# Kernel optimization log

Measured on AMD Instinct MI355X. Metric: run time of the kernel, lower is better.

The kernel has to match this reference:

```python
import jax, jax.numpy as jnp
import numpy as np

BATCH, CHANNELS, WINDOW, N_PATCHES = 16, 64, 200, 30
D_MODEL = 256
HIDDEN = D_MODEL // 2  # 128


def setup_inputs() -> dict:
    key = jax.random.key(0)
    ks = jax.random.split(key, 7)
    s = 1.0 / np.sqrt(HIDDEN)
    return {
        "x": jax.random.normal(ks[0], (BATCH, CHANNELS, WINDOW, N_PATCHES), dtype=jnp.float32),
        "W_ih": jax.random.normal(ks[1], (4 * HIDDEN, CHANNELS), dtype=jnp.float32) * s,
        "W_hh": jax.random.normal(ks[2], (4 * HIDDEN, HIDDEN), dtype=jnp.float32) * s,
        "b_ih": jax.random.normal(ks[3], (4 * HIDDEN,), dtype=jnp.float32) * s,
        "b_hh": jax.random.normal(ks[4], (4 * HIDDEN,), dtype=jnp.float32) * s,
        "W_fc": jax.random.normal(ks[5], (CHANNELS, HIDDEN), dtype=jnp.float32) * s,
        "b_fc": jax.random.normal(ks[6], (CHANNELS,), dtype=jnp.float32) * s,
    }


def _lstm_last_h(x_seq, W_ih, W_hh, b_ih, b_hh):
    # x_seq: (N, T, C) -> final hidden state (N, H). PyTorch gate order: i, f, g, o.
    N = x_seq.shape[0]
    H = W_hh.shape[1]
    # Precompute input contribution for all timesteps: (N, T, 4H)
    xg = jnp.einsum('ntc,gc->ntg', x_seq, W_ih) + b_ih + b_hh
    xg_t = jnp.swapaxes(xg, 0, 1)  # (T, N, 4H)

    def step(carry, xt):
        h, c = carry
        gates = xt + h @ W_hh.T  # (N, 4H)
        i, f, g, o = jnp.split(gates, 4, axis=-1)
        i = jax.nn.sigmoid(i)
        f = jax.nn.sigmoid(f)
        g = jnp.tanh(g)
        o = jax.nn.sigmoid(o)
        c = f * c + i * g
        h = o * jnp.tanh(c)
        return (h, c), None

    h0 = jnp.zeros((N, H), dtype=x_seq.dtype)
    c0 = jnp.zeros((N, H), dtype=x_seq.dtype)
    (h_T, _), _ = jax.lax.scan(step, (h0, c0), xg_t)
    return h_T


def reference(x, W_ih, W_hh, b_ih, b_hh, W_fc, b_fc):
    batch, channels, window, n_patches = x.shape
    # (B, C, T, P) -> (B, P, T, C) -> (B*P, T, C): each patch is an LSTM sequence
    x_flat = jnp.transpose(x, (0, 3, 2, 1)).reshape(batch * n_patches, window, channels)
    h_last = _lstm_last_h(x_flat, W_ih, W_hh, b_ih, b_hh)  # (B*P, H)
    out = h_last @ W_fc.T + b_fc  # (B*P, C)
    return out.reshape(batch, n_patches, channels)
```

## Files before the change

kernel.cpp:

```cpp
#include <hip/hip_runtime.h>

#define BATCH 16
#define CH    64
#define TLEN  200
#define NP    30
#define HID   128
#define NSEQ  (BATCH * NP)
#define HXP   136
#define XBP   72

typedef _Float16 half8  __attribute__((ext_vector_type(8)));
typedef _Float16 half4v __attribute__((ext_vector_type(4)));
typedef float    f32x4  __attribute__((ext_vector_type(4)));

__device__ __forceinline__ float sigm_fast(float x) {
    return __builtin_amdgcn_rcpf(1.0f + __expf(-x));
}
__device__ __forceinline__ float tanh_fast(float x) {
    float xc = fminf(15.0f, fmaxf(-15.0f, x));
    float e = __expf(2.0f * xc);
    return (e - 1.0f) * __builtin_amdgcn_rcpf(e + 1.0f);
}
__device__ __forceinline__ half8 cvt8(float4 a, float4 b) {
    return (half8){(_Float16)a.x,(_Float16)a.y,(_Float16)a.z,(_Float16)a.w,
                   (_Float16)b.x,(_Float16)b.y,(_Float16)b.z,(_Float16)b.w};
}

#define MFMA16(A,B,C) __builtin_amdgcn_mfma_f32_16x16x32_f16((A),(B),(C),0,0,0)

__global__ __launch_bounds__(512) void fused_lstm(
    const float* __restrict__ x, const float* __restrict__ W_ih,
    const float* __restrict__ W_hh, const float* __restrict__ b_ih,
    const float* __restrict__ b_hh, const float* __restrict__ W_fc,
    const float* __restrict__ b_fc, float* __restrict__ out)
{
    const int tid = threadIdx.x;
    const int w  = tid >> 6;
    const int l  = tid & 63;
    const int lr = l & 15;
    const int lq = l >> 4;

    const int n0 = blockIdx.x * 2;
    const int b0 = n0 / NP;
    const int p0 = n0 % NP;

    __shared__ __align__(16) _Float16 hx2[2][16][HXP];
    __shared__ __align__(16) _Float16 xbuf[2][16][XBP];
    __shared__ __align__(16) _Float16 xgb[2][8][HID][8];

    half8 bhh[4][4];
    half8 bih[4][2];
#pragma unroll
    for (int T = 0; T < 4; ++T) {
        const int g = 128*T + 16*w + lr;
        const float* rh = W_hh + (size_t)g * HID;
        const float* ri = W_ih + (size_t)g * CH;
#pragma unroll
        for (int kt = 0; kt < 4; ++kt) {
            const int k0 = 32*kt + 8*lq;
            bhh[T][kt] = cvt8(*(const float4*)(rh + k0), *(const float4*)(rh + k0 + 4));
        }
#pragma unroll
        for (int j = 0; j < 2; ++j) {
            const int k0 = 32*j + 8*lq;
            bih[T][j] = cvt8(*(const float4*)(ri + k0), *(const float4*)(ri + k0 + 4));
        }
    }
    float bias0, bias1, bias2, bias3;
    {
        const int gb = 16*w + lr;
        bias0 = b_ih[gb]       + b_hh[gb];
        bias1 = b_ih[gb + 128] + b_hh[gb + 128];
        bias2 = b_ih[gb + 256] + b_hh[gb + 256];
        bias3 = b_ih[gb + 384] + b_hh[gb + 384];
    }

    for (int i = tid; i < (2*16*HXP)/2; i += 512) ((unsigned*)hx2)[i] = 0u;

    const bool isload = (l >= 32 && l < 48);
    int ls = 0, lc = 0;
    const float* xbase = nullptr;
    float xpend = 0.f;
    if (isload) {
        const int idx = w * 16 + (l - 32);
        ls = idx >> 6;
        lc = idx & 63;
        xbase = x + ((size_t)(b0 * CH + lc) * TLEN) * NP + p0 + ls;
#pragma unroll
        for (int u = 0; u < 16; ++u)
            xbuf[u >> 3][2*(u & 7) + ls][lc] = (_Float16)xbase[(size_t)u * NP];
        xpend = xbase[(size_t)16 * NP];
    }
    float cst = 0.f;
    const int hcol = 16*w + lr;
    const int sq = lq & 1;
    __syncthreads();

#define XG_BURST(SB, TB) {                                                        \
        const _Float16* xr_ = &xbuf[SB][lr][8*lq];                                \
        half8 xf0_ = *(const half8*)xr_;                                          \
        half8 xf1_ = *(const half8*)(xr_ + 32);                                   \
        f32x4 x0_ = {bias0, bias0, bias0, bias0};                                 \
        f32x4 x1_ = {bias1, bias1, bias1, bias1};                                 \
        f32x4 x2_ = {bias2, bias2, bias2, bias2};                                 \
        f32x4 x3_ = {bias3, bias3, bias3, bias3};                                 \
        x0_ = MFMA16(xf0_, bih[0][0], x0_); x0_ = MFMA16(xf1_, bih[0][1], x0_);   \
        x1_ = MFMA16(xf0_, bih[1][0], x1_); x1_ = MFMA16(xf1_, bih[1][1], x1_);   \
        x2_ = MFMA16(xf0_, bih[2][0], x2_); x2_ = MFMA16(xf1_, bih[2][1], x2_);   \
        x3_ = MFMA16(xf0_, bih[3][0], x3_); x3_ = MFMA16(xf1_, bih[3][1], x3_);   \
        half8 r0_ = {(_Float16)x0_[0],(_Float16)x1_[0],(_Float16)x2_[0],(_Float16)x3_[0],  \
                     (_Float16)x0_[1],(_Float16)x1_[1],(_Float16)x2_[1],(_Float16)x3_[1]}; \
        half8 r1_ = {(_Float16)x0_[2],(_Float16)x1_[2],(_Float16)x2_[2],(_Float16)x3_[2],  \
                     (_Float16)x0_[3],(_Float16)x1_[3],(_Float16)x2_[3],(_Float16)x3_[3]}; \
        *(half8*)&xgb[TB][2*lq][hcol][0]     = r0_;                               \
        *(half8*)&xgb[TB][2*lq + 1][hcol][0] = r1_; }

    XG_BURST(0, 0)
    __syncthreads();

#define MM4(A, KT)                                                       \
        ci = MFMA16(A, bhh[0][KT], ci); cf = MFMA16(A, bhh[1][KT], cf);  \
        cg = MFMA16(A, bhh[2][KT], cg); co = MFMA16(A, bhh[3][KT], co);

#pragma unroll 1
    for (int p = 0; p < 25; ++p) {
        const int pe = p & 1;
#pragma unroll
        for (int k = 0; k < 8; ++k) {
            const int cur = k & 1;
            const int nxt = cur ^ 1;
            half4v xgv = *(const half4v*)&xgb[pe][k][hcol][4*sq];
            const _Float16* hr = &hx2[cur][lr][8*lq];
            half8 a0 = *(const half8*)(hr);
            half8 a1 = *(const half8*)(hr + 32);
            half8 a2 = *(const half8*)(hr + 64);
            half8 a3 = *(const half8*)(hr + 96);
            f32x4 ci = {0.f, 0.f, 0.f, 0.f};
            f32x4 cf = ci, cg = ci, co = ci;
            MM4(a0, 0) MM4(a1, 1) MM4(a2, 2) MM4(a3, 3)
            if (k == 0 && p < 24) XG_BURST(pe ^ 1, pe ^ 1)
            if (l < 32) {
                const bool lo = (l < 16);
                float gi = (lo ? ci[0] : ci[1]) + (float)xgv[0];
                float gf = (lo ? cf[0] : cf[1]) + (float)xgv[1];
                float gg = (lo ? cg[0] : cg[1]) + (float)xgv[2];
                float go = (lo ? co[0] : co[1]) + (float)xgv[3];
                cst = sigm_fast(gf) * cst + sigm_fast(gi) * tanh_fast(gg);
                float hv = sigm_fast(go) * tanh_fast(cst);
                _Float16 hh = (_Float16)hv;
                const int s_ = l >> 4;
                hx2[nxt][s_][hcol]     = hh;
                hx2[nxt][s_ + 4][hcol] = hh;
            } else if (isload) {
                xbuf[pe][2*k + ls][lc] = (_Float16)xpend;
                int tq = 8*p + k + 17;
                tq = tq > TLEN - 1 ? TLEN - 1 : tq;
                xpend = xbase[(size_t)tq * NP];
            }
            __syncthreads();
        }
    }

    if (tid < 2 * CH) {
        const int s = tid >> 6, ch = tid & 63;
        const float* wf = W_fc + (size_t)ch * HID;
        float acc = b_fc[ch];
#pragma unroll
        for (int j8 = 0; j8 < 16; ++j8) {
            half8 hv = *(const half8*)&hx2[0][s][8 * j8];
            float4 w0 = *(const float4*)(wf + 8 * j8);
            float4 w1 = *(const float4*)(wf + 8 * j8 + 4);
            acc += w0.x * (float)hv[0] + w0.y * (float)hv[1]
                 + w0.z * (float)hv[2] + w0.w * (float)hv[3]
                 + w1.x * (float)hv[4] + w1.y * (float)hv[5]
                 + w1.z * (float)hv[6] + w1.w * (float)hv[7];
        }
        out[(size_t)(n0 + s) * CH + ch] = acc;
    }
}

extern "C" void kernel_launch(void* const* d_in, const int* in_sizes, int n_in,
                              void* d_out, int out_size, void* d_ws, size_t ws_size,
                              hipStream_t stream) {
    (void)in_sizes; (void)n_in; (void)out_size; (void)d_ws; (void)ws_size;
    fused_lstm<<<NSEQ / 2, 512, 0, stream>>>(
        (const float*)d_in[0], (const float*)d_in[1], (const float*)d_in[2],
        (const float*)d_in[3], (const float*)d_in[4], (const float*)d_in[5],
        (const float*)d_in[6], (float*)d_out);
}
```

Measured before the change: 195.7 us.

## Halve block to 4 waves, each owning 32 hidden cells, with remapped block order

Shrinks the block from 8 to 4 wavefronts, so each wave holds recurrent and input weights for two 16-column hidden tiles and issues twice the MFMAs per step. All 64 lanes now do gate math (two sequences × 32 cells) instead of only half, and a dedicated set of threads handles x prefetch. The block index is permuted so consecutive blocks spread across the eight groups. The per-step barrier cost is meant to drop with fewer waves, at the cost of more VGPR pressure and a longer serial MFMA chain per wave.

```diff
diff --git a/kernel.cpp b/kernel.cpp
--- a/kernel.cpp
+++ b/kernel.cpp
@@ -28,7 +28,7 @@
 
 #define MFMA16(A,B,C) __builtin_amdgcn_mfma_f32_16x16x32_f16((A),(B),(C),0,0,0)
 
-__global__ __launch_bounds__(512) void fused_lstm(
+__global__ __launch_bounds__(256, 1) void fused_lstm(
     const float* __restrict__ x, const float* __restrict__ W_ih,
     const float* __restrict__ W_hh, const float* __restrict__ b_ih,
     const float* __restrict__ b_hh, const float* __restrict__ W_fc,
@@ -40,7 +40,9 @@
     const int lr = l & 15;
     const int lq = l >> 4;
 
-    const int n0 = blockIdx.x * 2;
+    const int blk  = blockIdx.x;
+    const int pair = (blk & 7) * 30 + (blk >> 3);
+    const int n0 = pair * 2;
     const int b0 = n0 / NP;
     const int p0 = n0 % NP;
 
@@ -48,43 +50,38 @@
     __shared__ __align__(16) _Float16 xbuf[2][16][XBP];
     __shared__ __align__(16) _Float16 xgb[2][8][HID][8];
 
-    half8 bhh[4][4];
-    half8 bih[4][2];
+    half8 bhh[4][2][4];
+    half8 bih[4][2][2];
+    float biasx[4][2];
 #pragma unroll
-    for (int T = 0; T < 4; ++T) {
-        const int g = 128*T + 16*w + lr;
+    for (int T = 0; T < 4; ++T)
+#pragma unroll
+      for (int ct = 0; ct < 2; ++ct) {
+        const int g = 128*T + 32*w + 16*ct + lr;
         const float* rh = W_hh + (size_t)g * HID;
         const float* ri = W_ih + (size_t)g * CH;
 #pragma unroll
         for (int kt = 0; kt < 4; ++kt) {
             const int k0 = 32*kt + 8*lq;
-            bhh[T][kt] = cvt8(*(const float4*)(rh + k0), *(const float4*)(rh + k0 + 4));
+            bhh[T][ct][kt] = cvt8(*(const float4*)(rh + k0), *(const float4*)(rh + k0 + 4));
         }
 #pragma unroll
         for (int j = 0; j < 2; ++j) {
             const int k0 = 32*j + 8*lq;
-            bih[T][j] = cvt8(*(const float4*)(ri + k0), *(const float4*)(ri + k0 + 4));
+            bih[T][ct][j] = cvt8(*(const float4*)(ri + k0), *(const float4*)(ri + k0 + 4));
         }
-    }
-    float bias0, bias1, bias2, bias3;
-    {
-        const int gb = 16*w + lr;
-        bias0 = b_ih[gb]       + b_hh[gb];
-        bias1 = b_ih[gb + 128] + b_hh[gb + 128];
-        bias2 = b_ih[gb + 256] + b_hh[gb + 256];
-        bias3 = b_ih[gb + 384] + b_hh[gb + 384];
-    }
+        biasx[T][ct] = b_ih[g] + b_hh[g];
+      }
 
-    for (int i = tid; i < (2*16*HXP)/2; i += 512) ((unsigned*)hx2)[i] = 0u;
+    for (int i = tid; i < (2*16*HXP)/2; i += 256) ((unsigned*)hx2)[i] = 0u;
 
-    const bool isload = (l >= 32 && l < 48);
+    const bool isload = (tid < 128);
     int ls = 0, lc = 0;
     const float* xbase = nullptr;
     float xpend = 0.f;
     if (isload) {
-        const int idx = w * 16 + (l - 32);
-        ls = idx >> 6;
-        lc = idx & 63;
+        ls = tid >> 6;
+        lc = tid & 63;
         xbase = x + ((size_t)(b0 * CH + lc) * TLEN) * NP + p0 + ls;
 #pragma unroll
         for (int u = 0; u < 16; ++u)
@@ -92,35 +89,39 @@
         xpend = xbase[(size_t)16 * NP];
     }
     float cst = 0.f;
-    const int hcol = 16*w + lr;
-    const int sq = lq & 1;
+    const int hcell = 32*w + (l & 31);
+    const int sb    = l >> 5;
+    const int ctb   = (l >> 4) & 1;
     __syncthreads();
 
 #define XG_BURST(SB, TB) {                                                        \
         const _Float16* xr_ = &xbuf[SB][lr][8*lq];                                \
         half8 xf0_ = *(const half8*)xr_;                                          \
         half8 xf1_ = *(const half8*)(xr_ + 32);                                   \
-        f32x4 x0_ = {bias0, bias0, bias0, bias0};                                 \
-        f32x4 x1_ = {bias1, bias1, bias1, bias1};                                 \
-        f32x4 x2_ = {bias2, bias2, bias2, bias2};                                 \
-        f32x4 x3_ = {bias3, bias3, bias3, bias3};                                 \
-        x0_ = MFMA16(xf0_, bih[0][0], x0_); x0_ = MFMA16(xf1_, bih[0][1], x0_);   \
-        x1_ = MFMA16(xf0_, bih[1][0], x1_); x1_ = MFMA16(xf1_, bih[1][1], x1_);   \
-        x2_ = MFMA16(xf0_, bih[2][0], x2_); x2_ = MFMA16(xf1_, bih[2][1], x2_);   \
-        x3_ = MFMA16(xf0_, bih[3][0], x3_); x3_ = MFMA16(xf1_, bih[3][1], x3_);   \
-        half8 r0_ = {(_Float16)x0_[0],(_Float16)x1_[0],(_Float16)x2_[0],(_Float16)x3_[0],  \
-                     (_Float16)x0_[1],(_Float16)x1_[1],(_Float16)x2_[1],(_Float16)x3_[1]}; \
-        half8 r1_ = {(_Float16)x0_[2],(_Float16)x1_[2],(_Float16)x2_[2],(_Float16)x3_[2],  \
-                     (_Float16)x0_[3],(_Float16)x1_[3],(_Float16)x2_[3],(_Float16)x3_[3]}; \
-        *(half8*)&xgb[TB][2*lq][hcol][0]     = r0_;                               \
-        *(half8*)&xgb[TB][2*lq + 1][hcol][0] = r1_; }
+        f32x4 xg_[4][2];                                                          \
+        _Pragma("unroll") for (int T_ = 0; T_ < 4; ++T_)                          \
+        { _Pragma("unroll") for (int c_ = 0; c_ < 2; ++c_) {                      \
+            f32x4 a_ = {biasx[T_][c_], biasx[T_][c_], biasx[T_][c_], biasx[T_][c_]}; \
+            a_ = MFMA16(xf0_, bih[T_][c_][0], a_);                                \
+            a_ = MFMA16(xf1_, bih[T_][c_][1], a_);                                \
+            xg_[T_][c_] = a_;                                                     \
+        } }                                                                       \
+        _Pragma("unroll") for (int c_ = 0; c_ < 2; ++c_) {                        \
+            const int hc_ = 32*w + 16*c_ + lr;                                    \
+            half8 r01_ = {(_Float16)xg_[0][c_][0],(_Float16)xg_[1][c_][0],        \
+                          (_Float16)xg_[2][c_][0],(_Float16)xg_[3][c_][0],        \
+                          (_Float16)xg_[0][c_][1],(_Float16)xg_[1][c_][1],        \
+                          (_Float16)xg_[2][c_][1],(_Float16)xg_[3][c_][1]};       \
+            half8 r23_ = {(_Float16)xg_[0][c_][2],(_Float16)xg_[1][c_][2],        \
+                          (_Float16)xg_[2][c_][2],(_Float16)xg_[3][c_][2],        \
+                          (_Float16)xg_[0][c_][3],(_Float16)xg_[1][c_][3],        \
+                          (_Float16)xg_[2][c_][3],(_Float16)xg_[3][c_][3]};       \
+            *(half8*)&xgb[TB][2*lq][hc_][0]     = r01_;                           \
+            *(half8*)&xgb[TB][2*lq + 1][hc_][0] = r23_;                           \
+        } }
 
     XG_BURST(0, 0)
     __syncthreads();
-
-#define MM4(A, KT)                                                       \
-        ci = MFMA16(A, bhh[0][KT], ci); cf = MFMA16(A, bhh[1][KT], cf);  \
-        cg = MFMA16(A, bhh[2][KT], cg); co = MFMA16(A, bhh[3][KT], co);
 
 #pragma unroll 1
     for (int p = 0; p < 25; ++p) {
@@ -129,33 +130,41 @@
         for (int k = 0; k < 8; ++k) {
             const int cur = k & 1;
             const int nxt = cur ^ 1;
-            half4v xgv = *(const half4v*)&xgb[pe][k][hcol][4*sq];
+            half4v xgv = *(const half4v*)&xgb[pe][k][hcell][4*sb];
             const _Float16* hr = &hx2[cur][lr][8*lq];
             half8 a0 = *(const half8*)(hr);
             half8 a1 = *(const half8*)(hr + 32);
             half8 a2 = *(const half8*)(hr + 64);
             half8 a3 = *(const half8*)(hr + 96);
-            f32x4 ci = {0.f, 0.f, 0.f, 0.f};
-            f32x4 cf = ci, cg = ci, co = ci;
-            MM4(a0, 0) MM4(a1, 1) MM4(a2, 2) MM4(a3, 3)
+            f32x4 acc[4][2];
+#pragma unroll
+            for (int T = 0; T < 4; ++T)
+#pragma unroll
+              for (int c = 0; c < 2; ++c) {
+                f32x4 z = {0.f, 0.f, 0.f, 0.f};
+                z = MFMA16(a0, bhh[T][c][0], z);
+                z = MFMA16(a1, bhh[T][c][1], z);
+                z = MFMA16(a2, bhh[T][c][2], z);
+                z = MFMA16(a3, bhh[T][c][3], z);
+                acc[T][c] = z;
+              }
             if (k == 0 && p < 24) XG_BURST(pe ^ 1, pe ^ 1)
-            if (l < 32) {
-                const bool lo = (l < 16);
-                float gi = (lo ? ci[0] : ci[1]) + (float)xgv[0];
-                float gf = (lo ? cf[0] : cf[1]) + (float)xgv[1];
-                float gg = (lo ? cg[0] : cg[1]) + (float)xgv[2];
-                float go = (lo ? co[0] : co[1]) + (float)xgv[3];
-                cst = sigm_fast(gf) * cst + sigm_fast(gi) * tanh_fast(gg);
-                float hv = sigm_fast(go) * tanh_fast(cst);
-                _Float16 hh = (_Float16)hv;
-                const int s_ = l >> 4;
-                hx2[nxt][s_][hcol]     = hh;
-                hx2[nxt][s_ + 4][hcol] = hh;
-            } else if (isload) {
+            if (isload) {
                 xbuf[pe][2*k + ls][lc] = (_Float16)xpend;
                 int tq = 8*p + k + 17;
                 tq = tq > TLEN - 1 ? TLEN - 1 : tq;
                 xpend = xbase[(size_t)tq * NP];
+            }
+            {
+                float gi = (ctb ? acc[0][1][0] : acc[0][0][0]) + (float)xgv[0];
+                float gf = (ctb ? acc[1][1][0] : acc[1][0][0]) + (float)xgv[1];
+                float gg = (ctb ? acc[2][1][0] : acc[2][0][0]) + (float)xgv[2];
+                float go = (ctb ? acc[3][1][0] : acc[3][0][0]) + (float)xgv[3];
+                cst = sigm_fast(gf) * cst + sigm_fast(gi) * tanh_fast(gg);
+                float hv = sigm_fast(go) * tanh_fast(cst);
+                _Float16 hh = (_Float16)hv;
+                hx2[nxt][8*sb][hcell]     = hh;
+                hx2[nxt][8*sb + 4][hcell] = hh;
             }
             __syncthreads();
         }
@@ -167,7 +176,7 @@
         float acc = b_fc[ch];
 #pragma unroll
         for (int j8 = 0; j8 < 16; ++j8) {
-            half8 hv = *(const half8*)&hx2[0][s][8 * j8];
+            half8 hv = *(const half8*)&hx2[0][8*s][8 * j8];
             float4 w0 = *(const float4*)(wf + 8 * j8);
             float4 w1 = *(const float4*)(wf + 8 * j8 + 4);
             acc += w0.x * (float)hv[0] + w0.y * (float)hv[1]
@@ -183,7 +192,7 @@
                               void* d_out, int out_size, void* d_ws, size_t ws_size,
                               hipStream_t stream) {
     (void)in_sizes; (void)n_in; (void)out_size; (void)d_ws; (void)ws_size;
-    fused_lstm<<<NSEQ / 2, 512, 0, stream>>>(
+    fused_lstm<<<NSEQ / 2, 256, 0, stream>>>(
         (const float*)d_in[0], (const float*)d_in[1], (const float*)d_in[2],
         (const float*)d_in[3], (const float*)d_in[4], (const float*)d_in[5],
         (const float*)d_in[6], (float*)d_out);
```

After: 200.1 us. 2.2% more time.

## Keep xgates in fp32, preload into MFMA accumulators, remap blocks and raise priority

Applied to the files above, without the earlier changes.

The precomputed input-gate values are now stored in LDS as fp32 in a padded per-row layout and used as the initial MFMA accumulators. This removes the separate add and select after the recurrent matmul and keeps the input contribution at full precision. Hidden-state rows are written to a new row mapping (4*lq), and the final FC reads from the matching rows. The block index is remapped to interleave sequence pairs, occupancy is hinted with launch_bounds(512,2), and s_setprio wraps the MFMA chain, at the cost of doubling the xgb LDS footprint.

```diff
diff --git a/kernel.cpp b/kernel.cpp
--- a/kernel.cpp
+++ b/kernel.cpp
@@ -8,10 +8,10 @@
 #define NSEQ  (BATCH * NP)
 #define HXP   136
 #define XBP   72
+#define XGW   520
 
-typedef _Float16 half8  __attribute__((ext_vector_type(8)));
-typedef _Float16 half4v __attribute__((ext_vector_type(4)));
-typedef float    f32x4  __attribute__((ext_vector_type(4)));
+typedef _Float16 half8 __attribute__((ext_vector_type(8)));
+typedef float    f32x4 __attribute__((ext_vector_type(4)));
 
 __device__ __forceinline__ float sigm_fast(float x) {
     return __builtin_amdgcn_rcpf(1.0f + __expf(-x));
@@ -28,7 +28,7 @@
 
 #define MFMA16(A,B,C) __builtin_amdgcn_mfma_f32_16x16x32_f16((A),(B),(C),0,0,0)
 
-__global__ __launch_bounds__(512) void fused_lstm(
+__global__ __launch_bounds__(512, 2) void fused_lstm(
     const float* __restrict__ x, const float* __restrict__ W_ih,
     const float* __restrict__ W_hh, const float* __restrict__ b_ih,
     const float* __restrict__ b_hh, const float* __restrict__ W_fc,
@@ -40,16 +40,19 @@
     const int lr = l & 15;
     const int lq = l >> 4;
 
-    const int n0 = blockIdx.x * 2;
+    const int blk  = blockIdx.x;
+    const int pair = (blk & 7) * 30 + (blk >> 3);
+    const int n0 = pair * 2;
     const int b0 = n0 / NP;
     const int p0 = n0 % NP;
 
     __shared__ __align__(16) _Float16 hx2[2][16][HXP];
     __shared__ __align__(16) _Float16 xbuf[2][16][XBP];
-    __shared__ __align__(16) _Float16 xgb[2][8][HID][8];
+    __shared__ __align__(16) float    xgb[2][16 * XGW];
 
     half8 bhh[4][4];
     half8 bih[4][2];
+    float biasx[4];
 #pragma unroll
     for (int T = 0; T < 4; ++T) {
         const int g = 128*T + 16*w + lr;
@@ -65,14 +68,7 @@
             const int k0 = 32*j + 8*lq;
             bih[T][j] = cvt8(*(const float4*)(ri + k0), *(const float4*)(ri + k0 + 4));
         }
-    }
-    float bias0, bias1, bias2, bias3;
-    {
-        const int gb = 16*w + lr;
-        bias0 = b_ih[gb]       + b_hh[gb];
-        bias1 = b_ih[gb + 128] + b_hh[gb + 128];
-        bias2 = b_ih[gb + 256] + b_hh[gb + 256];
-        bias3 = b_ih[gb + 384] + b_hh[gb + 384];
+        biasx[T] = b_ih[g] + b_hh[g];
     }
 
     for (int i = tid; i < (2*16*HXP)/2; i += 512) ((unsigned*)hx2)[i] = 0u;
@@ -93,34 +89,27 @@
     }
     float cst = 0.f;
     const int hcol = 16*w + lr;
-    const int sq = lq & 1;
     __syncthreads();
 
 #define XG_BURST(SB, TB) {                                                        \
         const _Float16* xr_ = &xbuf[SB][lr][8*lq];                                \
         half8 xf0_ = *(const half8*)xr_;                                          \
         half8 xf1_ = *(const half8*)(xr_ + 32);                                   \
-        f32x4 x0_ = {bias0, bias0, bias0, bias0};                                 \
-        f32x4 x1_ = {bias1, bias1, bias1, bias1};                                 \
-        f32x4 x2_ = {bias2, bias2, bias2, bias2};                                 \
-        f32x4 x3_ = {bias3, bias3, bias3, bias3};                                 \
-        x0_ = MFMA16(xf0_, bih[0][0], x0_); x0_ = MFMA16(xf1_, bih[0][1], x0_);   \
-        x1_ = MFMA16(xf0_, bih[1][0], x1_); x1_ = MFMA16(xf1_, bih[1][1], x1_);   \
-        x2_ = MFMA16(xf0_, bih[2][0], x2_); x2_ = MFMA16(xf1_, bih[2][1], x2_);   \
-        x3_ = MFMA16(xf0_, bih[3][0], x3_); x3_ = MFMA16(xf1_, bih[3][1], x3_);   \
-        half8 r0_ = {(_Float16)x0_[0],(_Float16)x1_[0],(_Float16)x2_[0],(_Float16)x3_[0],  \
-                     (_Float16)x0_[1],(_Float16)x1_[1],(_Float16)x2_[1],(_Float16)x3_[1]}; \
-        half8 r1_ = {(_Float16)x0_[2],(_Float16)x1_[2],(_Float16)x2_[2],(_Float16)x3_[2],  \
-                     (_Float16)x0_[3],(_Float16)x1_[3],(_Float16)x2_[3],(_Float16)x3_[3]}; \
-        *(half8*)&xgb[TB][2*lq][hcol][0]     = r0_;                               \
-        *(half8*)&xgb[TB][2*lq + 1][hcol][0] = r1_; }
+        f32x4 g0_ = {biasx[0], biasx[0], biasx[0], biasx[0]};                     \
+        f32x4 g1_ = {biasx[1], biasx[1], biasx[1], biasx[1]};                     \
+        f32x4 g2_ = {biasx[2], biasx[2], biasx[2], biasx[2]};                     \
+        f32x4 g3_ = {biasx[3], biasx[3], biasx[3], biasx[3]};                     \
+        g0_ = MFMA16(xf0_, bih[0][0], g0_); g0_ = MFMA16(xf1_, bih[0][1], g0_);   \
+        g1_ = MFMA16(xf0_, bih[1][0], g1_); g1_ = MFMA16(xf1_, bih[1][1], g1_);   \
+        g2_ = MFMA16(xf0_, bih[2][0], g2_); g2_ = MFMA16(xf1_, bih[2][1], g2_);   \
+        g3_ = MFMA16(xf0_, bih[3][0], g3_); g3_ = MFMA16(xf1_, bih[3][1], g3_);   \
+        _Pragma("unroll") for (int r_ = 0; r_ < 4; ++r_) {                        \
+            float* dst_ = &xgb[TB][(4*lq + r_) * XGW + hcol * 4];                 \
+            *(f32x4*)dst_ = (f32x4){g0_[r_], g1_[r_], g2_[r_], g3_[r_]};          \
+        } }
 
     XG_BURST(0, 0)
     __syncthreads();
-
-#define MM4(A, KT)                                                       \
-        ci = MFMA16(A, bhh[0][KT], ci); cf = MFMA16(A, bhh[1][KT], cf);  \
-        cg = MFMA16(A, bhh[2][KT], cg); co = MFMA16(A, bhh[3][KT], co);
 
 #pragma unroll 1
     for (int p = 0; p < 25; ++p) {
@@ -129,28 +118,31 @@
         for (int k = 0; k < 8; ++k) {
             const int cur = k & 1;
             const int nxt = cur ^ 1;
-            half4v xgv = *(const half4v*)&xgb[pe][k][hcol][4*sq];
+            f32x4 xg4 = *(const f32x4*)&xgb[pe][(2*k + (lq & 1)) * XGW + hcol * 4];
             const _Float16* hr = &hx2[cur][lr][8*lq];
             half8 a0 = *(const half8*)(hr);
             half8 a1 = *(const half8*)(hr + 32);
             half8 a2 = *(const half8*)(hr + 64);
             half8 a3 = *(const half8*)(hr + 96);
-            f32x4 ci = {0.f, 0.f, 0.f, 0.f};
-            f32x4 cf = ci, cg = ci, co = ci;
-            MM4(a0, 0) MM4(a1, 1) MM4(a2, 2) MM4(a3, 3)
+            f32x4 ci = xg4;
+            f32x4 cf = __builtin_shufflevector(xg4, xg4, 1, 1, 1, 1);
+            f32x4 cg = __builtin_shufflevector(xg4, xg4, 2, 2, 2, 2);
+            f32x4 co = __builtin_shufflevector(xg4, xg4, 3, 3, 3, 3);
+            __builtin_amdgcn_s_setprio(1);
+            ci = MFMA16(a0, bhh[0][0], ci); cf = MFMA16(a0, bhh[1][0], cf);
+            cg = MFMA16(a0, bhh[2][0], cg); co = MFMA16(a0, bhh[3][0], co);
+            ci = MFMA16(a1, bhh[0][1], ci); cf = MFMA16(a1, bhh[1][1], cf);
+            cg = MFMA16(a1, bhh[2][1], cg); co = MFMA16(a1, bhh[3][1], co);
+            ci = MFMA16(a2, bhh[0][2], ci); cf = MFMA16(a2, bhh[1][2], cf);
+            cg = MFMA16(a2, bhh[2][2], cg); co = MFMA16(a2, bhh[3][2], co);
+            ci = MFMA16(a3, bhh[0][3], ci); cf = MFMA16(a3, bhh[1][3], cf);
+            cg = MFMA16(a3, bhh[2][3], cg); co = MFMA16(a3, bhh[3][3], co);
+            __builtin_amdgcn_s_setprio(0);
             if (k == 0 && p < 24) XG_BURST(pe ^ 1, pe ^ 1)
             if (l < 32) {
-                const bool lo = (l < 16);
-                float gi = (lo ? ci[0] : ci[1]) + (float)xgv[0];
-                float gf = (lo ? cf[0] : cf[1]) + (float)xgv[1];
-                float gg = (lo ? cg[0] : cg[1]) + (float)xgv[2];
-                float go = (lo ? co[0] : co[1]) + (float)xgv[3];
-                cst = sigm_fast(gf) * cst + sigm_fast(gi) * tanh_fast(gg);
-                float hv = sigm_fast(go) * tanh_fast(cst);
-                _Float16 hh = (_Float16)hv;
-                const int s_ = l >> 4;
-                hx2[nxt][s_][hcol]     = hh;
-                hx2[nxt][s_ + 4][hcol] = hh;
+                cst = sigm_fast(cf[0]) * cst + sigm_fast(ci[0]) * tanh_fast(cg[0]);
+                float hv = sigm_fast(co[0]) * tanh_fast(cst);
+                hx2[nxt][4*lq][hcol] = (_Float16)hv;
             } else if (isload) {
                 xbuf[pe][2*k + ls][lc] = (_Float16)xpend;
                 int tq = 8*p + k + 17;
@@ -167,7 +159,7 @@
         float acc = b_fc[ch];
 #pragma unroll
         for (int j8 = 0; j8 < 16; ++j8) {
-            half8 hv = *(const half8*)&hx2[0][s][8 * j8];
+            half8 hv = *(const half8*)&hx2[0][4*s][8 * j8];
             float4 w0 = *(const float4*)(wf + 8 * j8);
             float4 w1 = *(const float4*)(wf + 8 * j8 + 4);
             acc += w0.x * (float)hv[0] + w0.y * (float)hv[1]
```

After: 195.6 us. About the same (-0.0%).
